# Performance work log

Measured on AMD Instinct MI355X. Metric: run time of the kernel, lower is better.

Reference implementation:

```python
import jax, jax.numpy as jnp
import numpy as np

E = 524288
B = 16
NODE_IN = 128
EDGE_IN = 64
GLOBAL_IN = 64
HIDDEN = 256
EDGE_OUT = 64
CAT_IN = EDGE_IN + 2 * NODE_IN + GLOBAL_IN  # 384


def setup_inputs() -> dict:
    key = jax.random.key(0)
    ks = jax.random.split(key, 9)
    src = jax.random.normal(ks[0], (E, NODE_IN), dtype=jnp.float32)
    dest = jax.random.normal(ks[1], (E, NODE_IN), dtype=jnp.float32)
    edge_attr = jax.random.normal(ks[2], (E, EDGE_IN), dtype=jnp.float32)
    u = jax.random.normal(ks[3], (B, GLOBAL_IN), dtype=jnp.float32)
    batch = jnp.sort(jax.random.randint(ks[4], (E,), 0, B, dtype=jnp.int64))
    # MLP params (torch Linear default init scale ~1/sqrt(fan_in))
    W1 = jax.random.normal(ks[5], (CAT_IN, HIDDEN), dtype=jnp.float32) / np.sqrt(CAT_IN)
    b1 = jax.random.normal(ks[6], (HIDDEN,), dtype=jnp.float32) / np.sqrt(CAT_IN)
    W2 = jax.random.normal(ks[7], (HIDDEN, EDGE_OUT), dtype=jnp.float32) / np.sqrt(HIDDEN)
    b2 = jax.random.normal(ks[8], (EDGE_OUT,), dtype=jnp.float32) / np.sqrt(HIDDEN)
    return {"src": src, "dest": dest, "edge_attr": edge_attr, "u": u,
            "batch": batch, "W1": W1, "b1": b1, "W2": W2, "b2": b2}


def reference(src, dest, edge_attr, u, batch, W1, b1, W2, b2):
    # gather global features per edge, concat, 2-layer MLP with ReLU
    x = jnp.concatenate([src, dest, edge_attr, u[batch]], axis=1)  # [E, 384]
    h = jax.nn.relu(x @ W1 + b1)                                   # [E, hidden]
    return h @ W2 + b2                                             # [E, edge_out]
```

## Files before the change

kernel.cpp:

```cpp
#include <hip/hip_runtime.h>

typedef __bf16 bf16_t;
typedef bf16_t bf16x8 __attribute__((ext_vector_type(8)));
typedef bf16_t bf16x4 __attribute__((ext_vector_type(4)));
typedef float f32x4 __attribute__((ext_vector_type(4)));
typedef unsigned short u16;
typedef unsigned int u32;

#define E_TOT 524288
#define MT 64
#define NBLK (E_TOT / MT)

__device__ __forceinline__ u16 f2bf(float f) {
  u32 u = __builtin_bit_cast(u32, f);
  u += 0x7FFFu + ((u >> 16) & 1u);
  return (u16)(u >> 16);
}

__device__ __forceinline__ bf16x8 pack8(f32x4 a, f32x4 b) {
  bf16x8 p;
  p[0] = (bf16_t)a[0]; p[1] = (bf16_t)a[1]; p[2] = (bf16_t)a[2]; p[3] = (bf16_t)a[3];
  p[4] = (bf16_t)b[0]; p[5] = (bf16_t)b[1]; p[6] = (bf16_t)b[2]; p[7] = (bf16_t)b[3];
  return p;
}

__device__ __forceinline__ void gload_lds16(const void* g, void* l) {
  __builtin_amdgcn_global_load_lds(
      (const __attribute__((address_space(1))) u32*)g,
      (__attribute__((address_space(3))) u32*)l, 16, 0, 0);
}

__global__ void prep_w1tc(const float* __restrict__ W1, u16* __restrict__ W1Tc) {
  int t = blockIdx.x * 256 + threadIdx.x;
  if (t < 384 * 256) {
    int U = t >> 3, e = t & 7;
    int c = U >> 10, rem = U & 1023;
    int n = rem >> 2, j = rem & 3;
    int k = c * 32 + ((j ^ ((n >> 1) & 3)) << 3) + e;
    W1Tc[t] = f2bf(W1[k * 256 + n]);
  }
}

__global__ void prep_w2f(const float* __restrict__ W2, u16* __restrict__ W2F) {
  int t = blockIdx.x * 256 + threadIdx.x;
  if (t < 16384) {
    int e   = t & 7;
    int l   = (t >> 3) & 63;
    int n2f = (t >> 9) & 3;
    int ks  = t >> 11;
    int n2 = n2f * 16 + (l & 15);
    int k  = ks * 32 + ((l >> 4) << 3) + e;
    W2F[t] = f2bf(W2[k * 64 + n2]);
  }
}

__global__ void __launch_bounds__(256) edge_fused(
    const float* __restrict__ src, const float* __restrict__ dst,
    const float* __restrict__ ea, const float* __restrict__ u,
    const int* __restrict__ batch, const u16* __restrict__ W1Tc,
    const float* __restrict__ b1, const u16* __restrict__ W2F,
    const float* __restrict__ b2, float* __restrict__ out)
{
  __shared__ __align__(16) u16 smem[20480];
  u16* As = smem;
  u16* Wb = smem + 4096;
  u16* Hs = smem;

  const int t    = threadIdx.x;
  const int wid  = t >> 6;
  const int lane = t & 63;
  const int lr   = lane & 15;
  const int lg   = lane >> 4;
  const int e0   = blockIdx.x * MT;
  const int r    = t >> 2;
  const int jcol = t & 3;
  const int bidx = batch[e0 + r];
  const int wunit = r * 4 + (jcol ^ ((r >> 1) & 3));

  auto loadA = [&](int c, f32x4* ra) {
    const float* p;
    if (c < 4)       p = src + (size_t)(e0 + r) * 128 + c * 32 + jcol * 8;
    else if (c < 8)  p = dst + (size_t)(e0 + r) * 128 + (c - 4) * 32 + jcol * 8;
    else if (c < 10) p = ea + (size_t)(e0 + r) * 64 + (c - 8) * 32 + jcol * 8;
    else             p = u + (size_t)bidx * 64 + (c - 10) * 32 + jcol * 8;
    ra[0] = *(const f32x4*)p;
    ra[1] = *(const f32x4*)(p + 4);
  };
  auto issueW = [&](int c, u16* Wn) {
    #pragma unroll
    for (int g = 0; g < 4; ++g) {
      int ub = wid * 256 + g * 64;
      gload_lds16(W1Tc + ((size_t)c * 1024 + ub + lane) * 8, Wn + ub * 8);
    }
  };

  f32x4 a0[2], a1[2], a2[2];
  loadA(0, a0);
  loadA(1, a1);
  loadA(2, a2);
  issueW(0, Wb);
  issueW(1, Wb + 8192);

  f32x4 acc[4][4];
  #pragma unroll
  for (int i = 0; i < 4; ++i)
    #pragma unroll
    for (int j = 0; j < 4; ++j)
      acc[i][j] = (f32x4){0.f, 0.f, 0.f, 0.f};

  #pragma unroll
  for (int kb = 0; kb < 12; ++kb) {
    f32x4* cur = (kb % 3 == 0) ? a0 : (kb % 3 == 1) ? a1 : a2;
    u16* Ab = As + (kb & 1) * 2048;
    u16* Wc = Wb + (kb & 1) * 8192;

    *(bf16x8*)&Ab[wunit * 8] = pack8(cur[0], cur[1]);
    if (kb <= 8) loadA(kb + 3, cur);

    if (kb == 0)       asm volatile("s_waitcnt vmcnt(6) lgkmcnt(0)" ::: "memory");
    else if (kb <= 8)  asm volatile("s_waitcnt vmcnt(8) lgkmcnt(0)" ::: "memory");
    else if (kb == 9)  asm volatile("s_waitcnt vmcnt(6) lgkmcnt(0)" ::: "memory");
    else if (kb == 10) asm volatile("s_waitcnt vmcnt(4) lgkmcnt(0)" ::: "memory");
    else               asm volatile("s_waitcnt vmcnt(0) lgkmcnt(0)" ::: "memory");
    __builtin_amdgcn_sched_barrier(0);
    __builtin_amdgcn_s_barrier();

    __builtin_amdgcn_s_setprio(1);
    bf16x8 af[4];
    #pragma unroll
    for (int mf = 0; mf < 4; ++mf) {
      int row = mf * 16 + lr;
      af[mf] = *(const bf16x8*)&Ab[(row * 4 + (lg ^ ((row >> 1) & 3))) * 8];
    }
    #pragma unroll
    for (int nf = 0; nf < 4; ++nf) {
      int n = wid * 64 + nf * 16 + lr;
      bf16x8 wfr = *(const bf16x8*)&Wc[(n * 4 + (lg ^ ((n >> 1) & 3))) * 8];
      #pragma unroll
      for (int mf = 0; mf < 4; ++mf)
        acc[nf][mf] = __builtin_amdgcn_mfma_f32_16x16x32_bf16(wfr, af[mf], acc[nf][mf], 0, 0, 0);
    }
    __builtin_amdgcn_s_setprio(0);
    __builtin_amdgcn_s_barrier();

    if (kb <= 9) issueW(kb + 2, Wc);
  }

  #pragma unroll
  for (int nf = 0; nf < 4; ++nf) {
    f32x4 b1v = *(const f32x4*)(b1 + wid * 64 + nf * 16 + lg * 4);
    #pragma unroll
    for (int mf = 0; mf < 4; ++mf) {
      int row = mf * 16 + lr;
      bf16x4 hb;
      #pragma unroll
      for (int rr = 0; rr < 4; ++rr)
        hb[rr] = (bf16_t)fmaxf(acc[nf][mf][rr] + b1v[rr], 0.f);
      int uu = (wid * 4 + nf) * 4 + lg;
      int up = uu ^ ((lr & 3) << 2);
      *(bf16x4*)&Hs[row * 256 + up * 4] = hb;
    }
  }
  __syncthreads();

  const int row2 = wid * 16 + lr;
  f32x4 d2[4];
  #pragma unroll
  for (int i = 0; i < 4; ++i) d2[i] = (f32x4){0.f, 0.f, 0.f, 0.f};
  #pragma unroll
  for (int ks = 0; ks < 8; ++ks) {
    int uu = ks * 8 + lg * 2;
    int up = uu ^ ((lr & 3) << 2);
    bf16x8 a2 = *(const bf16x8*)&Hs[row2 * 256 + up * 4];
    const u16* q = W2F + (size_t)ks * 2048 + lane * 8;
    #pragma unroll
    for (int n2f = 0; n2f < 4; ++n2f)
      d2[n2f] = __builtin_amdgcn_mfma_f32_16x16x32_bf16(
          *(const bf16x8*)(q + n2f * 512), a2, d2[n2f], 0, 0, 0);
  }

  #pragma unroll
  for (int n2f = 0; n2f < 4; ++n2f) {
    f32x4 b2v = *(const f32x4*)(b2 + n2f * 16 + lg * 4);
    f32x4 ov = d2[n2f] + b2v;
    *(f32x4*)&out[(size_t)(e0 + row2) * 64 + n2f * 16 + lg * 4] = ov;
  }
}

extern "C" void kernel_launch(void* const* d_in, const int* in_sizes, int n_in,
                              void* d_out, int out_size, void* d_ws, size_t ws_size,
                              hipStream_t stream) {
  const float* src  = (const float*)d_in[0];
  const float* dst  = (const float*)d_in[1];
  const float* ea   = (const float*)d_in[2];
  const float* u    = (const float*)d_in[3];
  const int* batch  = (const int*)d_in[4];
  const float* W1   = (const float*)d_in[5];
  const float* b1   = (const float*)d_in[6];
  const float* W2   = (const float*)d_in[7];
  const float* b2   = (const float*)d_in[8];
  float* out = (float*)d_out;

  u16* W1Tc = (u16*)d_ws;
  u16* W2F  = W1Tc + 384 * 256;

  prep_w1tc<<<(384 * 256 + 255) / 256, 256, 0, stream>>>(W1, W1Tc);
  prep_w2f<<<64, 256, 0, stream>>>(W2, W2F);
  edge_fused<<<NBLK, 256, 0, stream>>>(src, dst, ea, u, batch, W1Tc, b1, W2F, b2, out);
}
```

Measured before the change: 256.9 us.

## Stream fp32 activations directly into LDS via async global_load_lds

Result: no change. 257.8 us (+0.4%).

```diff
diff --git a/kernel.cpp b/kernel.cpp
--- a/kernel.cpp
+++ b/kernel.cpp
@@ -61,10 +61,10 @@
     const float* __restrict__ b1, const u16* __restrict__ W2F,
     const float* __restrict__ b2, float* __restrict__ out)
 {
-  __shared__ __align__(16) u16 smem[20480];
-  u16* As = smem;
-  u16* Wb = smem + 4096;
-  u16* Hs = smem;
+  __shared__ __align__(16) u16 smem[24576];
+  float* Af = (float*)smem;
+  u16*   Wb = smem + 8192;
+  u16*   Hs = smem;
 
   const int t    = threadIdx.x;
   const int wid  = t >> 6;
@@ -72,19 +72,30 @@
   const int lr   = lane & 15;
   const int lg   = lane >> 4;
   const int e0   = blockIdx.x * MT;
-  const int r    = t >> 2;
-  const int jcol = t & 3;
-  const int bidx = batch[e0 + r];
-  const int wunit = r * 4 + (jcol ^ ((r >> 1) & 3));
-
-  auto loadA = [&](int c, f32x4* ra) {
-    const float* p;
-    if (c < 4)       p = src + (size_t)(e0 + r) * 128 + c * 32 + jcol * 8;
-    else if (c < 8)  p = dst + (size_t)(e0 + r) * 128 + (c - 4) * 32 + jcol * 8;
-    else if (c < 10) p = ea + (size_t)(e0 + r) * 64 + (c - 8) * 32 + jcol * 8;
-    else             p = u + (size_t)bidx * 64 + (c - 10) * 32 + jcol * 8;
-    ra[0] = *(const f32x4*)p;
-    ra[1] = *(const f32x4*)(p + 4);
+
+  const int rl   = lane >> 3;
+  const int jl   = lane & 7;
+  const int rowA = wid * 16 + rl;
+  const int rowB = rowA + 8;
+  const int sjA  = jl ^ (rowA & 7);
+  const int sjB  = jl ^ (rowB & 7);
+  const float* psrcA = src + (size_t)(e0 + rowA) * 128 + sjA * 4;
+  const float* psrcB = src + (size_t)(e0 + rowB) * 128 + sjB * 4;
+  const float* pdstA = dst + (size_t)(e0 + rowA) * 128 + sjA * 4;
+  const float* pdstB = dst + (size_t)(e0 + rowB) * 128 + sjB * 4;
+  const float* peaA  = ea + (size_t)(e0 + rowA) * 64 + sjA * 4;
+  const float* peaB  = ea + (size_t)(e0 + rowB) * 64 + sjB * 4;
+  const float* puA   = u + (size_t)batch[e0 + rowA] * 64 + sjA * 4;
+  const float* puB   = u + (size_t)batch[e0 + rowB] * 64 + sjB * 4;
+
+  auto issueA = [&](int c, float* Ad) {
+    const float *qa, *qb;
+    if (c < 4)       { qa = psrcA + c * 32;       qb = psrcB + c * 32; }
+    else if (c < 8)  { qa = pdstA + (c - 4) * 32; qb = pdstB + (c - 4) * 32; }
+    else if (c < 10) { qa = peaA + (c - 8) * 32;  qb = peaB + (c - 8) * 32; }
+    else             { qa = puA + (c - 10) * 32;  qb = puB + (c - 10) * 32; }
+    gload_lds16(qa, Ad + wid * 512);
+    gload_lds16(qb, Ad + wid * 512 + 256);
   };
   auto issueW = [&](int c, u16* Wn) {
     #pragma unroll
@@ -94,12 +105,8 @@
     }
   };
 
-  f32x4 a0[2], a1[2], a2[2];
-  loadA(0, a0);
-  loadA(1, a1);
-  loadA(2, a2);
-  issueW(0, Wb);
-  issueW(1, Wb + 8192);
+  issueA(0, Af);        issueW(0, Wb);
+  issueA(1, Af + 2048); issueW(1, Wb + 8192);
 
   f32x4 acc[4][4];
   #pragma unroll
@@ -110,18 +117,11 @@
 
   #pragma unroll
   for (int kb = 0; kb < 12; ++kb) {
-    f32x4* cur = (kb % 3 == 0) ? a0 : (kb % 3 == 1) ? a1 : a2;
-    u16* Ab = As + (kb & 1) * 2048;
+    const float* Ac = Af + (kb & 1) * 2048;
     u16* Wc = Wb + (kb & 1) * 8192;
 
-    *(bf16x8*)&Ab[wunit * 8] = pack8(cur[0], cur[1]);
-    if (kb <= 8) loadA(kb + 3, cur);
-
-    if (kb == 0)       asm volatile("s_waitcnt vmcnt(6) lgkmcnt(0)" ::: "memory");
-    else if (kb <= 8)  asm volatile("s_waitcnt vmcnt(8) lgkmcnt(0)" ::: "memory");
-    else if (kb == 9)  asm volatile("s_waitcnt vmcnt(6) lgkmcnt(0)" ::: "memory");
-    else if (kb == 10) asm volatile("s_waitcnt vmcnt(4) lgkmcnt(0)" ::: "memory");
-    else               asm volatile("s_waitcnt vmcnt(0) lgkmcnt(0)" ::: "memory");
+    if (kb < 11) asm volatile("s_waitcnt vmcnt(6)" ::: "memory");
+    else         asm volatile("s_waitcnt vmcnt(0)" ::: "memory");
     __builtin_amdgcn_sched_barrier(0);
     __builtin_amdgcn_s_barrier();
 
@@ -130,7 +130,9 @@
     #pragma unroll
     for (int mf = 0; mf < 4; ++mf) {
       int row = mf * 16 + lr;
-      af[mf] = *(const bf16x8*)&Ab[(row * 4 + (lg ^ ((row >> 1) & 3))) * 8];
+      f32x4 v0 = *(const f32x4*)(Ac + row * 32 + (((2 * lg)     ^ (row & 7)) << 2));
+      f32x4 v1 = *(const f32x4*)(Ac + row * 32 + (((2 * lg + 1) ^ (row & 7)) << 2));
+      af[mf] = pack8(v0, v1);
     }
     #pragma unroll
     for (int nf = 0; nf < 4; ++nf) {
@@ -141,9 +143,15 @@
         acc[nf][mf] = __builtin_amdgcn_mfma_f32_16x16x32_bf16(wfr, af[mf], acc[nf][mf], 0, 0, 0);
     }
     __builtin_amdgcn_s_setprio(0);
+
+    asm volatile("s_waitcnt lgkmcnt(0)" ::: "memory");
     __builtin_amdgcn_s_barrier();
-
-    if (kb <= 9) issueW(kb + 2, Wc);
+    __builtin_amdgcn_sched_barrier(0);
+
+    if (kb <= 9) {
+      issueA(kb + 2, Af + (kb & 1) * 2048);
+      issueW(kb + 2, Wb + (kb & 1) * 8192);
+    }
   }
 
   #pragma unroll
@@ -161,7 +169,9 @@
       *(bf16x4*)&Hs[row * 256 + up * 4] = hb;
     }
   }
-  __syncthreads();
+  asm volatile("s_waitcnt lgkmcnt(0)" ::: "memory");
+  __builtin_amdgcn_s_barrier();
+  __builtin_amdgcn_sched_barrier(0);
 
   const int row2 = wid * 16 + lr;
   f32x4 d2[4];
```
